# Kernel tuning notes

Hardware: AMD Instinct MI355X
Metric: run time of the kernel (lower is better)

The kernel has to match this reference:

```python
import jax, jax.numpy as jnp
import numpy as np

B, N, F_IN, F_OUT, K = 4, 8192, 32, 64, 4


def setup_inputs() -> dict:
    key = jax.random.key(0)
    k0, k1, k2, k3 = jax.random.split(key, 4)
    x = jax.random.normal(k0, (B, N, F_IN), dtype=jnp.float32)
    # dense rescaled-Laplacian-like symmetric operator, spectrally ~O(1)
    A = jax.random.normal(k1, (N, N), dtype=jnp.float32) / np.float32(np.sqrt(N))
    L = 0.5 * (A + A.T)
    stdv = np.float32(1.0 / np.sqrt(F_IN * K))  # matches uniform(in_channels*K, .)
    weight = jax.random.uniform(k2, (K, F_IN, F_OUT), dtype=jnp.float32, minval=-stdv, maxval=stdv)
    bias = jax.random.uniform(k3, (1, N, F_OUT), dtype=jnp.float32, minval=-stdv, maxval=stdv)
    return {"x": x, "L": L, "weight": weight, "bias": bias}


def _chebyshev(L, x, K):
    # Faithful to the torch code: X is overwritten by L @ X each step (matrix
    # powers), and Xt[k] = 2 * L^k x - Xt[k-2]. This is NOT the textbook
    # Chebyshev recurrence, but it is what the module computes.
    Xt = [x]
    X = x
    if K > 1:
        X = jnp.einsum('ab,cbe->cae', L, X)  # [B,N,F]
        Xt.append(X)
    for k in range(2, K):
        X = jnp.einsum('ab,cbe->cae', L, X)
        Xt.append(2.0 * X - Xt[k - 2])
    return jnp.stack(Xt)  # [K,B,N,F]


def reference(x, L, weight, bias):
    Kdim = weight.shape[0]
    xc = _chebyshev(L, x, Kdim)                       # [K,B,N,F]
    out = jnp.einsum('abcd,ade->bce', xc, weight)     # contract K and F_in
    return out + bias                                 # [B,N,F_out]
```

## Files before the change

kernel.cpp:

```cpp
#include <hip/hip_runtime.h>


typedef __bf16 bf16;
typedef bf16 bf16x8 __attribute__((ext_vector_type(8)));
typedef bf16 bf16x4 __attribute__((ext_vector_type(4)));
typedef float f32x4 __attribute__((ext_vector_type(4)));

static_assert(sizeof(bf16x8) == 16, "bf16x8 must be 16B");

#define N_DIM 8192
#define NCOLS 128
#define BM 128
#define BK 64
#define SPLITS 8
#define KCHUNK (N_DIM / SPLITS)

__device__ inline unsigned short f2bf_bits(float f) {
    bf16 b = (bf16)f;
    return __builtin_bit_cast(unsigned short, b);
}

__device__ inline void load_lds16(const bf16* g, bf16* l) {
    __builtin_amdgcn_global_load_lds(
        (const __attribute__((address_space(1))) void*)g,
        (__attribute__((address_space(3))) void*)l, 16, 0, 0);
}

__global__ __launch_bounds__(256) void convert_L_kernel(
    const float* __restrict__ L, bf16* __restrict__ Lb) {
    size_t i = ((size_t)blockIdx.x * 256 + threadIdx.x) * 4;
    const float4 v = *(const float4*)(L + i);
    bf16x4 p;
    p[0] = (bf16)v.x; p[1] = (bf16)v.y; p[2] = (bf16)v.z; p[3] = (bf16)v.w;
    *(bf16x4*)(Lb + i) = p;
}

__global__ __launch_bounds__(256) void pack_x_kernel(
    const float* __restrict__ x, bf16* __restrict__ Xb0) {
    int g = blockIdx.x * 256 + threadIdx.x;
    int n = g & 8191;
    int c = g >> 13;
    int b = c >> 5, fi = c & 31;
    Xb0[(size_t)c * N_DIM + n] = (bf16)x[((size_t)b * N_DIM + n) * 32 + fi];
}

__global__ __launch_bounds__(256) void init_out_kernel(
    const float* __restrict__ x, const float* __restrict__ w,
    const float* __restrict__ bias, float* __restrict__ out) {
    __shared__ float weff0[32 * 64];
    __shared__ float xs[16 * 32];
    int t = threadIdx.x;
    for (int i = t; i < 2048; i += 256) weff0[i] = w[i] - w[2 * 2048 + i];
    int r0 = blockIdx.x * 16;
    for (int i = t; i < 512; i += 256) {
        int lr = i >> 5, fi = i & 31;
        xs[i] = x[(size_t)(r0 + lr) * 32 + fi];
    }
    __syncthreads();
    for (int i = t; i < 1024; i += 256) {
        int lr = i >> 6, fo = i & 63;
        int r = r0 + lr;
        float acc = bias[(size_t)(r & 8191) * 64 + fo];
#pragma unroll
        for (int fi = 0; fi < 32; fi++)
            acc += xs[lr * 32 + fi] * weff0[fi * 64 + fo];
        out[(size_t)r * 64 + fo] = acc;
    }
}

__global__ __launch_bounds__(256, 2) void gemm_kernel(
    const bf16* __restrict__ Lb, const bf16* __restrict__ Xb,
    float* __restrict__ part) {
    __shared__ bf16 As[BM * BK];
    __shared__ bf16 Bs[NCOLS * BK];

    const int mt = blockIdx.x;
    const int sp = blockIdx.y;
    const int rbase = mt * BM;
    const size_t kbase = (size_t)sp * KCHUNK;
    const int t = threadIdx.x;
    const int lane = t & 63;
    const int wave = t >> 6;
    const int wr = wave >> 1, wc = wave & 1;
    const int lm = lane & 15, kq = lane >> 4;

    const int lrow = lane >> 3;
    const int jb = (lane & 7) ^ lrow;

    f32x4 acc[4][4];
    const f32x4 zero = {0.f, 0.f, 0.f, 0.f};
#pragma unroll
    for (int mi = 0; mi < 4; mi++)
#pragma unroll
        for (int ni = 0; ni < 4; ni++) acc[mi][ni] = zero;

    for (int kk = 0; kk < KCHUNK; kk += BK) {
#pragma unroll
        for (int i = 0; i < 4; i++) {
            const int c = wave * 4 + i;
            const int row = 8 * c + lrow;
            load_lds16(&Lb[(size_t)(rbase + row) * N_DIM + kbase + kk + jb * 8],
                       &As[c * 512]);
            load_lds16(&Xb[(size_t)row * N_DIM + kbase + kk + jb * 8],
                       &Bs[c * 512]);
        }
        __syncthreads();

#pragma unroll
        for (int ks = 0; ks < 2; ks++) {
            bf16x8 af[4], bfr[4];
#pragma unroll
            for (int mi = 0; mi < 4; mi++) {
                int r = wr * 64 + mi * 16 + lm;
                int cb = (kq + 4 * ks) ^ (lm & 7);
                af[mi] = *(const bf16x8*)(&As[r * BK + cb * 8]);
            }
#pragma unroll
            for (int ni = 0; ni < 4; ni++) {
                int r = wc * 64 + ni * 16 + lm;
                int cb = (kq + 4 * ks) ^ (lm & 7);
                bfr[ni] = *(const bf16x8*)(&Bs[r * BK + cb * 8]);
            }
#pragma unroll
            for (int mi = 0; mi < 4; mi++)
#pragma unroll
                for (int ni = 0; ni < 4; ni++)
                    acc[mi][ni] = __builtin_amdgcn_mfma_f32_16x16x32_bf16(
                        af[mi], bfr[ni], acc[mi][ni], 0, 0, 0);
        }
        __syncthreads();
    }

    float* P = part + (size_t)sp * N_DIM * NCOLS;
#pragma unroll
    for (int mi = 0; mi < 4; mi++) {
        int row0 = rbase + wr * 64 + mi * 16 + kq * 4;
#pragma unroll
        for (int ni = 0; ni < 4; ni++) {
            int col = wc * 64 + ni * 16 + lm;
#pragma unroll
            for (int r = 0; r < 4; r++)
                P[(size_t)(row0 + r) * NCOLS + col] = acc[mi][ni][r];
        }
    }
}

__global__ __launch_bounds__(256) void combine_kernel(
    const float* __restrict__ part, const float* __restrict__ w,
    float* __restrict__ out, bf16* __restrict__ XbNext, int pass) {
    __shared__ float Yt[128 * 66];
    __shared__ float weff[32 * 64];
    int t = threadIdx.x;
    int n0 = blockIdx.x * 64;

    for (int i = t; i < 2048; i += 256) {
        float v;
        if (pass == 1)      v = w[1 * 2048 + i] - w[3 * 2048 + i];
        else if (pass == 2) v = 2.f * w[2 * 2048 + i];
        else                v = 2.f * w[3 * 2048 + i];
        weff[i] = v;
    }
    for (int slot = t; slot < 2048; slot += 256) {
        int row = slot >> 5;
        int c4 = slot & 31;
        float4 s = {0.f, 0.f, 0.f, 0.f};
#pragma unroll
        for (int sp = 0; sp < SPLITS; sp++) {
            const float4 v = *(const float4*)(
                &part[(size_t)sp * N_DIM * NCOLS + (size_t)(n0 + row) * NCOLS + c4 * 4]);
            s.x += v.x; s.y += v.y; s.z += v.z; s.w += v.w;
        }
        Yt[(c4 * 4 + 0) * 66 + row] = s.x;
        Yt[(c4 * 4 + 1) * 66 + row] = s.y;
        Yt[(c4 * 4 + 2) * 66 + row] = s.z;
        Yt[(c4 * 4 + 3) * 66 + row] = s.w;
    }
    __syncthreads();
    if (pass < 3) {
        int c = t >> 1;
        int nh = (t & 1) * 32;
#pragma unroll
        for (int v4 = 0; v4 < 4; v4++) {
            union { uint4 u; unsigned short s[8]; } pk;
#pragma unroll
            for (int j = 0; j < 8; j++)
                pk.s[j] = f2bf_bits(Yt[c * 66 + nh + v4 * 8 + j]);
            *(uint4*)(&XbNext[(size_t)c * N_DIM + n0 + nh + v4 * 8]) = pk.u;
        }
    }
    int b = t >> 6, fo = t & 63;
    for (int n = 0; n < 64; n++) {
        size_t oidx = ((size_t)b * N_DIM + n0 + n) * 64 + fo;
        float accv = out[oidx];
#pragma unroll
        for (int fi = 0; fi < 32; fi++)
            accv += Yt[(b * 32 + fi) * 66 + n] * weff[fi * 64 + fo];
        out[oidx] = accv;
    }
}

extern "C" void kernel_launch(void* const* d_in, const int* in_sizes, int n_in,
                              void* d_out, int out_size, void* d_ws, size_t ws_size,
                              hipStream_t stream) {
    const float* x    = (const float*)d_in[0];
    const float* L    = (const float*)d_in[1];
    const float* w    = (const float*)d_in[2];
    const float* bias = (const float*)d_in[3];
    float* out = (float*)d_out;

    char* ws = (char*)d_ws;
    bf16* Lb   = (bf16*)ws;
    bf16* XbA  = (bf16*)(ws + (128ull << 20));
    bf16* XbB  = (bf16*)(ws + (130ull << 20));
    float* part = (float*)(ws + (132ull << 20));

    convert_L_kernel<<<(N_DIM * (size_t)N_DIM) / (4 * 256), 256, 0, stream>>>(L, Lb);
    pack_x_kernel<<<(NCOLS * N_DIM) / 256, 256, 0, stream>>>(x, XbA);
    init_out_kernel<<<(4 * N_DIM) / 16, 256, 0, stream>>>(x, w, bias, out);

    dim3 ggrid(N_DIM / BM, SPLITS);
    gemm_kernel<<<ggrid, 256, 0, stream>>>(Lb, XbA, part);
    combine_kernel<<<N_DIM / 64, 256, 0, stream>>>(part, w, out, XbB, 1);
    gemm_kernel<<<ggrid, 256, 0, stream>>>(Lb, XbB, part);
    combine_kernel<<<N_DIM / 64, 256, 0, stream>>>(part, w, out, XbA, 2);
    gemm_kernel<<<ggrid, 256, 0, stream>>>(Lb, XbA, part);
    combine_kernel<<<N_DIM / 64, 256, 0, stream>>>(part, w, out, XbA, 3);
}
```

Measured before the change: 545.1 us.

## Fuse all passes into one persistent kernel with grid-wide barriers

```diff
diff --git a/kernel.cpp b/kernel.cpp
--- a/kernel.cpp
+++ b/kernel.cpp
@@ -2,8 +2,8 @@
 
 
 typedef __bf16 bf16;
+typedef bf16 bf16x4 __attribute__((ext_vector_type(4)));
 typedef bf16 bf16x8 __attribute__((ext_vector_type(8)));
-typedef bf16 bf16x4 __attribute__((ext_vector_type(4)));
 typedef float f32x4 __attribute__((ext_vector_type(4)));
 
 static_assert(sizeof(bf16x8) == 16, "bf16x8 must be 16B");
@@ -14,6 +14,8 @@
 #define BK 64
 #define SPLITS 8
 #define KCHUNK (N_DIM / SPLITS)
+#define NWG 512
+#define NT 256
 
 __device__ inline unsigned short f2bf_bits(float f) {
     bf16 b = (bf16)f;
@@ -26,64 +28,35 @@
         (__attribute__((address_space(3))) void*)l, 16, 0, 0);
 }
 
-__global__ __launch_bounds__(256) void convert_L_kernel(
-    const float* __restrict__ L, bf16* __restrict__ Lb) {
-    size_t i = ((size_t)blockIdx.x * 256 + threadIdx.x) * 4;
-    const float4 v = *(const float4*)(L + i);
-    bf16x4 p;
-    p[0] = (bf16)v.x; p[1] = (bf16)v.y; p[2] = (bf16)v.z; p[3] = (bf16)v.w;
-    *(bf16x4*)(Lb + i) = p;
-}
-
-__global__ __launch_bounds__(256) void pack_x_kernel(
-    const float* __restrict__ x, bf16* __restrict__ Xb0) {
-    int g = blockIdx.x * 256 + threadIdx.x;
-    int n = g & 8191;
-    int c = g >> 13;
-    int b = c >> 5, fi = c & 31;
-    Xb0[(size_t)c * N_DIM + n] = (bf16)x[((size_t)b * N_DIM + n) * 32 + fi];
-}
-
-__global__ __launch_bounds__(256) void init_out_kernel(
-    const float* __restrict__ x, const float* __restrict__ w,
-    const float* __restrict__ bias, float* __restrict__ out) {
-    __shared__ float weff0[32 * 64];
-    __shared__ float xs[16 * 32];
-    int t = threadIdx.x;
-    for (int i = t; i < 2048; i += 256) weff0[i] = w[i] - w[2 * 2048 + i];
-    int r0 = blockIdx.x * 16;
-    for (int i = t; i < 512; i += 256) {
-        int lr = i >> 5, fi = i & 31;
-        xs[i] = x[(size_t)(r0 + lr) * 32 + fi];
-    }
+__global__ void zero_cnt_kernel(int* cnt) {
+    if (threadIdx.x < 16) cnt[threadIdx.x] = 0;
+}
+
+__device__ inline void grid_barrier(int* cnt, int idx) {
     __syncthreads();
-    for (int i = t; i < 1024; i += 256) {
-        int lr = i >> 6, fo = i & 63;
-        int r = r0 + lr;
-        float acc = bias[(size_t)(r & 8191) * 64 + fo];
-#pragma unroll
-        for (int fi = 0; fi < 32; fi++)
-            acc += xs[lr * 32 + fi] * weff0[fi * 64 + fo];
-        out[(size_t)r * 64 + fo] = acc;
-    }
-}
-
-__global__ __launch_bounds__(256, 2) void gemm_kernel(
+    if (threadIdx.x == 0) {
+        __threadfence();
+        __hip_atomic_fetch_add(&cnt[idx], 1, __ATOMIC_ACQ_REL,
+                               __HIP_MEMORY_SCOPE_AGENT);
+        while (__hip_atomic_load(&cnt[idx], __ATOMIC_ACQUIRE,
+                                 __HIP_MEMORY_SCOPE_AGENT) < NWG)
+            __builtin_amdgcn_s_sleep(2);
+        __threadfence();
+    }
+    __syncthreads();
+}
+
+__device__ __attribute__((always_inline)) void gemm_phase(
     const bf16* __restrict__ Lb, const bf16* __restrict__ Xb,
-    float* __restrict__ part) {
-    __shared__ bf16 As[BM * BK];
-    __shared__ bf16 Bs[NCOLS * BK];
-
-    const int mt = blockIdx.x;
-    const int sp = blockIdx.y;
+    float* __restrict__ part, bf16* As, bf16* Bs, int wg, int t) {
+    const int mt = wg & 63;
+    const int sp = wg >> 6;
     const int rbase = mt * BM;
     const size_t kbase = (size_t)sp * KCHUNK;
-    const int t = threadIdx.x;
     const int lane = t & 63;
     const int wave = t >> 6;
     const int wr = wave >> 1, wc = wave & 1;
     const int lm = lane & 15, kq = lane >> 4;
-
     const int lrow = lane >> 3;
     const int jb = (lane & 7) ^ lrow;
 
@@ -145,58 +118,118 @@
     }
 }
 
-__global__ __launch_bounds__(256) void combine_kernel(
+__device__ __attribute__((always_inline)) void combine_phase(
     const float* __restrict__ part, const float* __restrict__ w,
-    float* __restrict__ out, bf16* __restrict__ XbNext, int pass) {
-    __shared__ float Yt[128 * 66];
-    __shared__ float weff[32 * 64];
-    int t = threadIdx.x;
-    int n0 = blockIdx.x * 64;
-
-    for (int i = t; i < 2048; i += 256) {
+    float* __restrict__ out, bf16* __restrict__ XbNext,
+    float* weff, float* Yt, int pass, int wg, int t) {
+    const int n0 = wg * 16;
+
+    for (int i = t; i < 2048; i += NT) {
         float v;
-        if (pass == 1)      v = w[1 * 2048 + i] - w[3 * 2048 + i];
+        if (pass == 1)      v = w[2048 + i] - w[3 * 2048 + i];
         else if (pass == 2) v = 2.f * w[2 * 2048 + i];
         else                v = 2.f * w[3 * 2048 + i];
         weff[i] = v;
     }
-    for (int slot = t; slot < 2048; slot += 256) {
-        int row = slot >> 5;
-        int c4 = slot & 31;
-        float4 s = {0.f, 0.f, 0.f, 0.f};
+    for (int s = t; s < 512; s += NT) {
+        int row = s >> 5, c4 = s & 31;
+        float4 sum = {0.f, 0.f, 0.f, 0.f};
 #pragma unroll
         for (int sp = 0; sp < SPLITS; sp++) {
             const float4 v = *(const float4*)(
                 &part[(size_t)sp * N_DIM * NCOLS + (size_t)(n0 + row) * NCOLS + c4 * 4]);
-            s.x += v.x; s.y += v.y; s.z += v.z; s.w += v.w;
-        }
-        Yt[(c4 * 4 + 0) * 66 + row] = s.x;
-        Yt[(c4 * 4 + 1) * 66 + row] = s.y;
-        Yt[(c4 * 4 + 2) * 66 + row] = s.z;
-        Yt[(c4 * 4 + 3) * 66 + row] = s.w;
+            sum.x += v.x; sum.y += v.y; sum.z += v.z; sum.w += v.w;
+        }
+        Yt[(c4 * 4 + 0) * 17 + row] = sum.x;
+        Yt[(c4 * 4 + 1) * 17 + row] = sum.y;
+        Yt[(c4 * 4 + 2) * 17 + row] = sum.z;
+        Yt[(c4 * 4 + 3) * 17 + row] = sum.w;
     }
     __syncthreads();
     if (pass < 3) {
-        int c = t >> 1;
-        int nh = (t & 1) * 32;
-#pragma unroll
-        for (int v4 = 0; v4 < 4; v4++) {
-            union { uint4 u; unsigned short s[8]; } pk;
-#pragma unroll
-            for (int j = 0; j < 8; j++)
-                pk.s[j] = f2bf_bits(Yt[c * 66 + nh + v4 * 8 + j]);
-            *(uint4*)(&XbNext[(size_t)c * N_DIM + n0 + nh + v4 * 8]) = pk.u;
-        }
+        int c = t >> 1, half = t & 1;
+        union { uint4 u; unsigned short s[8]; } pk;
+#pragma unroll
+        for (int j = 0; j < 8; j++)
+            pk.s[j] = f2bf_bits(Yt[c * 17 + half * 8 + j]);
+        *(uint4*)(&XbNext[(size_t)c * N_DIM + n0 + half * 8]) = pk.u;
     }
     int b = t >> 6, fo = t & 63;
-    for (int n = 0; n < 64; n++) {
+    for (int n = 0; n < 16; n++) {
         size_t oidx = ((size_t)b * N_DIM + n0 + n) * 64 + fo;
-        float accv = out[oidx];
+        float acc = out[oidx];
 #pragma unroll
         for (int fi = 0; fi < 32; fi++)
-            accv += Yt[(b * 32 + fi) * 66 + n] * weff[fi * 64 + fo];
-        out[oidx] = accv;
-    }
+            acc += Yt[(b * 32 + fi) * 17 + n] * weff[fi * 64 + fo];
+        out[oidx] = acc;
+    }
+}
+
+__global__ __launch_bounds__(256, 2) void fused_kernel(
+    const float* __restrict__ L, const float* __restrict__ x,
+    const float* __restrict__ w, const float* __restrict__ bias,
+    float* __restrict__ out, bf16* __restrict__ Lb,
+    bf16* __restrict__ XbA, bf16* __restrict__ XbB,
+    float* __restrict__ part, int* __restrict__ cnt) {
+    __shared__ alignas(16) unsigned char smem[32768];
+    const int wg = blockIdx.x, t = threadIdx.x;
+
+    {
+        const float4* Lf4 = (const float4*)L;
+        const size_t base = (size_t)wg * NT + t;
+#pragma unroll 4
+        for (int i = 0; i < 128; i++) {
+            size_t idx = base + (size_t)i * (NWG * NT);
+            float4 v = Lf4[idx];
+            bf16x4 p;
+            p[0] = (bf16)v.x; p[1] = (bf16)v.y; p[2] = (bf16)v.z; p[3] = (bf16)v.w;
+            *(bf16x4*)(Lb + idx * 4) = p;
+        }
+#pragma unroll
+        for (int i = 0; i < 8; i++) {
+            size_t g = base + (size_t)i * (NWG * NT);
+            int n = (int)(g & 8191), c = (int)(g >> 13);
+            int b = c >> 5, fi = c & 31;
+            XbA[(size_t)c * N_DIM + n] = (bf16)x[((size_t)b * N_DIM + n) * 32 + fi];
+        }
+    }
+    {
+        float* weff0 = (float*)smem;
+        float* xs = (float*)(smem + 8192);
+        const int n0 = wg * 16;
+        for (int i = t; i < 2048; i += NT) weff0[i] = w[i] - w[2 * 2048 + i];
+        for (int i = t; i < 2048; i += NT) {
+            int b = i >> 9, lr = (i >> 5) & 15, fi = i & 31;
+            xs[i] = x[((size_t)b * N_DIM + n0 + lr) * 32 + fi];
+        }
+        __syncthreads();
+        int b = t >> 6, fo = t & 63;
+        for (int n = 0; n < 16; n++) {
+            float acc = bias[(size_t)(n0 + n) * 64 + fo];
+#pragma unroll
+            for (int fi = 0; fi < 32; fi++)
+                acc += xs[b * 512 + n * 32 + fi] * weff0[fi * 64 + fo];
+            out[((size_t)b * N_DIM + n0 + n) * 64 + fo] = acc;
+        }
+    }
+    grid_barrier(cnt, 0);
+
+    bf16* As = (bf16*)smem;
+    bf16* Bs = (bf16*)(smem + 16384);
+    float* weff = (float*)smem;
+    float* Yt = (float*)(smem + 8192);
+
+    gemm_phase(Lb, XbA, part, As, Bs, wg, t);
+    grid_barrier(cnt, 1);
+    combine_phase(part, w, out, XbB, weff, Yt, 1, wg, t);
+    grid_barrier(cnt, 2);
+    gemm_phase(Lb, XbB, part, As, Bs, wg, t);
+    grid_barrier(cnt, 3);
+    combine_phase(part, w, out, XbA, weff, Yt, 2, wg, t);
+    grid_barrier(cnt, 4);
+    gemm_phase(Lb, XbA, part, As, Bs, wg, t);
+    grid_barrier(cnt, 5);
+    combine_phase(part, w, out, XbA, weff, Yt, 3, wg, t);
 }
 
 extern "C" void kernel_launch(void* const* d_in, const int* in_sizes, int n_in,
@@ -209,20 +242,12 @@
     float* out = (float*)d_out;
 
     char* ws = (char*)d_ws;
-    bf16* Lb   = (bf16*)ws;
-    bf16* XbA  = (bf16*)(ws + (128ull << 20));
-    bf16* XbB  = (bf16*)(ws + (130ull << 20));
+    bf16* Lb    = (bf16*)ws;
+    bf16* XbA   = (bf16*)(ws + (128ull << 20));
+    bf16* XbB   = (bf16*)(ws + (130ull << 20));
     float* part = (float*)(ws + (132ull << 20));
-
-    convert_L_kernel<<<(N_DIM * (size_t)N_DIM) / (4 * 256), 256, 0, stream>>>(L, Lb);
-    pack_x_kernel<<<(NCOLS * N_DIM) / 256, 256, 0, stream>>>(x, XbA);
-    init_out_kernel<<<(4 * N_DIM) / 16, 256, 0, stream>>>(x, w, bias, out);
-
-    dim3 ggrid(N_DIM / BM, SPLITS);
-    gemm_kernel<<<ggrid, 256, 0, stream>>>(Lb, XbA, part);
-    combine_kernel<<<N_DIM / 64, 256, 0, stream>>>(part, w, out, XbB, 1);
-    gemm_kernel<<<ggrid, 256, 0, stream>>>(Lb, XbB, part);
-    combine_kernel<<<N_DIM / 64, 256, 0, stream>>>(part, w, out, XbA, 2);
-    gemm_kernel<<<ggrid, 256, 0, stream>>>(Lb, XbA, part);
-    combine_kernel<<<N_DIM / 64, 256, 0, stream>>>(part, w, out, XbA, 3);
-}
+    int* cnt    = (int*)(ws + (164ull << 20));
+
+    zero_cnt_kernel<<<1, 64, 0, stream>>>(cnt);
+    fused_kernel<<<NWG, NT, 0, stream>>>(L, x, w, bias, out, Lb, XbA, XbB, part, cnt);
+}
```

New measurement: 1.102 ms. +102.2%, slower.

## Stream L fragments directly from global into registers, stage only X in LDS

Applied to the files above, without the earlier changes.

```diff
diff --git a/kernel.cpp b/kernel.cpp
--- a/kernel.cpp
+++ b/kernel.cpp
@@ -2,8 +2,8 @@
 
 
 typedef __bf16 bf16;
+typedef bf16 bf16x4 __attribute__((ext_vector_type(4)));
 typedef bf16 bf16x8 __attribute__((ext_vector_type(8)));
-typedef bf16 bf16x4 __attribute__((ext_vector_type(4)));
 typedef float f32x4 __attribute__((ext_vector_type(4)));
 
 static_assert(sizeof(bf16x8) == 16, "bf16x8 must be 16B");
@@ -11,9 +11,9 @@
 #define N_DIM 8192
 #define NCOLS 128
 #define BM 128
-#define BK 64
 #define SPLITS 8
 #define KCHUNK (N_DIM / SPLITS)
+#define SUBK 256
 
 __device__ inline unsigned short f2bf_bits(float f) {
     bf16 b = (bf16)f;
@@ -71,73 +71,65 @@
 __global__ __launch_bounds__(256, 2) void gemm_kernel(
     const bf16* __restrict__ Lb, const bf16* __restrict__ Xb,
     float* __restrict__ part) {
-    __shared__ bf16 As[BM * BK];
-    __shared__ bf16 Bs[NCOLS * BK];
+    __shared__ bf16 Bs[NCOLS * SUBK];
 
     const int mt = blockIdx.x;
     const int sp = blockIdx.y;
     const int rbase = mt * BM;
-    const size_t kbase = (size_t)sp * KCHUNK;
     const int t = threadIdx.x;
     const int lane = t & 63;
     const int wave = t >> 6;
-    const int wr = wave >> 1, wc = wave & 1;
     const int lm = lane & 15, kq = lane >> 4;
-
-    const int lrow = lane >> 3;
-    const int jb = (lane & 7) ^ lrow;
-
-    f32x4 acc[4][4];
+    const int scol2 = lane >> 5;
+    const int skb = lane & 31;
+
+    f32x4 acc[2][8];
     const f32x4 zero = {0.f, 0.f, 0.f, 0.f};
 #pragma unroll
-    for (int mi = 0; mi < 4; mi++)
-#pragma unroll
-        for (int ni = 0; ni < 4; ni++) acc[mi][ni] = zero;
-
-    for (int kk = 0; kk < KCHUNK; kk += BK) {
-#pragma unroll
-        for (int i = 0; i < 4; i++) {
-            const int c = wave * 4 + i;
-            const int row = 8 * c + lrow;
-            load_lds16(&Lb[(size_t)(rbase + row) * N_DIM + kbase + kk + jb * 8],
-                       &As[c * 512]);
-            load_lds16(&Xb[(size_t)row * N_DIM + kbase + kk + jb * 8],
-                       &Bs[c * 512]);
+    for (int mi = 0; mi < 2; mi++)
+#pragma unroll
+        for (int ni = 0; ni < 8; ni++) acc[mi][ni] = zero;
+
+    const bf16* Arow0 = Lb + (size_t)(rbase + wave * 32 + lm) * N_DIM;
+    const bf16* Arow1 = Lb + (size_t)(rbase + wave * 32 + 16 + lm) * N_DIM;
+
+    for (int sc = 0; sc < KCHUNK / SUBK; sc++) {
+        const size_t kb = (size_t)sp * KCHUNK + sc * SUBK;
+#pragma unroll
+        for (int i = 0; i < 16; i++) {
+            int c = wave * 16 + i;
+            int col = 2 * c + scol2;
+            int klog = skb ^ (col & 7);
+            load_lds16(&Xb[(size_t)col * N_DIM + kb + klog * 8], &Bs[c * 512]);
         }
         __syncthreads();
 
-#pragma unroll
-        for (int ks = 0; ks < 2; ks++) {
-            bf16x8 af[4], bfr[4];
-#pragma unroll
-            for (int mi = 0; mi < 4; mi++) {
-                int r = wr * 64 + mi * 16 + lm;
-                int cb = (kq + 4 * ks) ^ (lm & 7);
-                af[mi] = *(const bf16x8*)(&As[r * BK + cb * 8]);
+#pragma unroll 4
+        for (int st = 0; st < 8; st++) {
+            const size_t ko = kb + st * 32 + kq * 8;
+            bf16x8 a0 = *(const bf16x8*)(Arow0 + ko);
+            bf16x8 a1 = *(const bf16x8*)(Arow1 + ko);
+#pragma unroll
+            for (int ni = 0; ni < 8; ni++) {
+                int col = ni * 16 + lm;
+                int kphys = (st * 4 + kq) ^ (col & 7);
+                bf16x8 bfrag = *(const bf16x8*)(&Bs[col * SUBK + kphys * 8]);
+                acc[0][ni] = __builtin_amdgcn_mfma_f32_16x16x32_bf16(
+                    a0, bfrag, acc[0][ni], 0, 0, 0);
+                acc[1][ni] = __builtin_amdgcn_mfma_f32_16x16x32_bf16(
+                    a1, bfrag, acc[1][ni], 0, 0, 0);
             }
-#pragma unroll
-            for (int ni = 0; ni < 4; ni++) {
-                int r = wc * 64 + ni * 16 + lm;
-                int cb = (kq + 4 * ks) ^ (lm & 7);
-                bfr[ni] = *(const bf16x8*)(&Bs[r * BK + cb * 8]);
-            }
-#pragma unroll
-            for (int mi = 0; mi < 4; mi++)
-#pragma unroll
-                for (int ni = 0; ni < 4; ni++)
-                    acc[mi][ni] = __builtin_amdgcn_mfma_f32_16x16x32_bf16(
-                        af[mi], bfr[ni], acc[mi][ni], 0, 0, 0);
         }
         __syncthreads();
     }
 
     float* P = part + (size_t)sp * N_DIM * NCOLS;
 #pragma unroll
-    for (int mi = 0; mi < 4; mi++) {
-        int row0 = rbase + wr * 64 + mi * 16 + kq * 4;
-#pragma unroll
-        for (int ni = 0; ni < 4; ni++) {
-            int col = wc * 64 + ni * 16 + lm;
+    for (int mi = 0; mi < 2; mi++) {
+        int row0 = rbase + wave * 32 + mi * 16 + kq * 4;
+#pragma unroll
+        for (int ni = 0; ni < 8; ni++) {
+            int col = ni * 16 + lm;
 #pragma unroll
             for (int r = 0; r < 4; r++)
                 P[(size_t)(row0 + r) * NCOLS + col] = acc[mi][ni][r];
@@ -155,7 +147,7 @@
 
     for (int i = t; i < 2048; i += 256) {
         float v;
-        if (pass == 1)      v = w[1 * 2048 + i] - w[3 * 2048 + i];
+        if (pass == 1)      v = w[2048 + i] - w[3 * 2048 + i];
         else if (pass == 2) v = 2.f * w[2 * 2048 + i];
         else                v = 2.f * w[3 * 2048 + i];
         weff[i] = v;
```

Result: no change. 551.6 us (+1.2%).
